# Kernel tuning notes

Hardware: AMD Instinct MI355X
Metric: run time of the kernel (lower is better)

## Reference

```python
import jax, jax.numpy as jnp
import numpy as np

V, L, H, D = 2048, 16, 8, 64   # vocab, max_chars, n_head, word_vec_d
B = 8192                        # number of words in batch (rows of char_code)
NW_TOTAL = 8192                 # len(word_code)
N_NAMES = 2048                  # total names (4 words each)
N_GROUPS = 8                    # groups of names (256 each)
PAD = 0
TEMP = D ** 0.5
LN_EPS = 1e-5


def make_pos():
    freq = D // 2
    inv = 1.0 / np.power(10000.0, np.arange(freq) / freq)
    ph = np.outer(np.arange(L), inv)
    return jnp.asarray(np.hstack([np.cos(ph), np.sin(ph)]).astype(np.float32))


def setup_inputs() -> dict:
    key = jax.random.key(0)
    ks = jax.random.split(key, 8)
    char_emb = jax.random.normal(ks[0], (V, D), jnp.float32) * 0.02
    char_emb = char_emb.at[PAD].set(0.0)  # padding_idx row
    Wc = jax.random.normal(ks[1], (D, 3 * H * D), jnp.float32) * 0.02
    bc = jnp.zeros((3 * H * D,), jnp.float32)
    Wp = jax.random.normal(ks[2], (D, 3 * H * D), jnp.float32) * 0.02
    bp = jnp.zeros((3 * H * D,), jnp.float32)
    gamma = jnp.ones((D,), jnp.float32)
    beta = jnp.zeros((D,), jnp.float32)
    W1 = jax.random.normal(ks[3], (H, 16), jnp.float32) * 0.1
    b1 = jnp.zeros((16,), jnp.float32)
    W2 = jax.random.normal(ks[4], (16, 8), jnp.float32) * 0.1
    b2 = jnp.zeros((8,), jnp.float32)
    char_code = jax.random.randint(ks[5], (B, L), 1, V)
    char_code = char_code.at[::4, -2:].set(PAD)  # some padded tails
    word_code = jax.random.randint(ks[6], (NW_TOTAL,), 0, B)
    n_words = np.full((N_NAMES,), NW_TOTAL // N_NAMES, dtype=np.int64)
    n_names = np.full((N_GROUPS,), N_NAMES // N_GROUPS, dtype=np.int64)
    return {"char_emb": char_emb, "Wc": Wc, "bc": bc, "Wp": Wp, "bp": bp,
            "gamma": gamma, "beta": beta, "W1": W1, "b1": b1, "W2": W2, "b2": b2,
            "char_code": char_code, "word_code": word_code,
            "n_words": n_words, "n_names": n_names}


def reference(char_emb, Wc, bc, Wp, bp, gamma, beta, W1, b1, W2, b2,
              char_code, word_code, n_words, n_names):
    pos = make_pos()
    # ComputeQKV: linear d -> 3*H*d, reshape [N,3,H,D]
    cqkv = (char_emb @ Wc + bc).reshape(V, 3, H, D)
    cq, ck, cv = cqkv[:, 0], cqkv[:, 1], cqkv[:, 2]        # [V,H,D]
    pqkv = (pos @ Wp + bp).reshape(L, 3, H, D)
    pq, pk, pv = pqkv[:, 0], pqkv[:, 1], pqkv[:, 2]        # [L,H,D]
    # precomputed score tables
    char_qk = jnp.einsum('xhd,yhd->hxy', cq, ck).at[:, :, PAD].set(-1e9)  # [H,V,V]
    pos_qk = jnp.einsum('xhd,yhd->hxy', pq, pk)                            # [H,L,L]
    # char_q@pos_k + (pos_q@char_k)^T summed over the first dim of char_pos_qk
    cp = jnp.einsum('vhd,lhd->hvl', cq, pk) + jnp.einsum('lhd,vhd->hvl', pq, ck)  # [H,V,L]
    code = char_code                                        # [B,L]
    # gather-assembled scores, no [H,B*L,V] intermediate
    sim = (char_qk[:, code[:, :, None], code[:, None, :]]   # [H,B,L,L]
           + cp[:, code]
           + pos_qk[:, None]) / TEMP
    attn = jax.nn.softmax(sim, axis=-1)                     # [H,B,L,L] (dropout=0)
    v = jnp.transpose(cv[code], (2, 0, 1, 3)) + pv.transpose(1, 0, 2)[:, None]  # [H,B,L,D]
    out = jnp.einsum('hbij,hbjd->bihd', attn, v)            # [B,L,H,D]
    mu = out.mean(-1, keepdims=True)
    var = out.var(-1, keepdims=True)
    out = (out - mu) / jnp.sqrt(var + LN_EPS) * gamma + beta  # LayerNorm(D)
    char_ft = jnp.transpose(out, (0, 2, 1, 3))              # [B,H,L,D]
    mask = (code != PAD)
    pooled = jnp.einsum('bl,bhld->bhd', mask.astype(out.dtype), char_ft) \
             / mask.sum(-1)[:, None, None]                  # masked mean over chars
    x = jnp.transpose(pooled, (0, 2, 1))                    # [B,D,H]
    x = jax.nn.relu(x @ W1 + b1) @ W2 + b2                  # MLP over head dim -> [B,D,8]
    word_ft = x.reshape(B, -1)[word_code]                   # [NW_TOTAL, D*8]
    nw = np.asarray(n_words)
    seg = jnp.asarray(np.repeat(np.arange(nw.size), nw))
    name_ft = jax.ops.segment_sum(word_ft, seg, num_segments=nw.size) \
              / jnp.asarray(nw, word_ft.dtype)[:, None]     # ragged mean -> [N_NAMES, D*8]
    splits = np.cumsum(np.asarray(n_names))[:-1]
    return tuple(jnp.split(name_ft, splits, axis=0))
```

## Files before the change

### kernel.cpp

```cpp
#include <hip/hip_runtime.h>
#include <hip/hip_bf16.h>
#include <math.h>

typedef __attribute__((ext_vector_type(8))) short bfrag;
typedef __attribute__((ext_vector_type(4))) float ffrag;
typedef __attribute__((ext_vector_type(4))) float f4v;

#define C3 1536
#define PS 24

__device__ __forceinline__ unsigned short f2bf(float f) {
    unsigned u = __float_as_uint(f);
    return (unsigned short)((u + 0x7FFFu + ((u >> 16) & 1u)) >> 16);
}
__device__ __forceinline__ float bf2f(unsigned short s) {
    return __uint_as_float(((unsigned)s) << 16);
}

__global__ __launch_bounds__(256) void precompute_kernel(
    const float* __restrict__ char_emb, const float* __restrict__ Wc, const float* __restrict__ bc,
    const float* __restrict__ Wp, const float* __restrict__ bp,
    unsigned short* __restrict__ cqkv, float* __restrict__ pqkv,
    unsigned short* __restrict__ pbf)
{
    const int b = blockIdx.x;
    const int t = threadIdx.x;
    if (b < 1536) {
        const int mt = b / 6;
        const int nt = b - mt * 6;
        const int m0 = mt * 8;
        const int c = nt * 256 + t;
        const float bias = bc[c];
        float acc[8];
        #pragma unroll
        for (int r = 0; r < 8; ++r) acc[r] = bias;
        #pragma unroll 16
        for (int dd = 0; dd < 64; ++dd) {
            const float wv = Wc[dd * C3 + c];
            #pragma unroll
            for (int r = 0; r < 8; ++r)
                acc[r] = fmaf(char_emb[(m0 + r) * 64 + dd], wv, acc[r]);
        }
        #pragma unroll
        for (int r = 0; r < 8; ++r)
            cqkv[(size_t)(m0 + r) * C3 + c] = f2bf(acc[r]);
    } else {
        const int l = b - 1536;
        __shared__ float spos[64];
        if (t < 64) {
            const int f = t & 31;
            const float inv = exp2f(-(float)f * 0.41524101186092034f);
            const float ph = (float)l * inv;
            spos[t] = (t < 32) ? cosf(ph) : sinf(ph);
        }
        __syncthreads();
        #pragma unroll
        for (int cc = 0; cc < 6; ++cc) {
            const int c = t + cc * 256;
            float acc = bp[c];
            #pragma unroll
            for (int dd = 0; dd < 64; ++dd)
                acc = fmaf(spos[dd], Wp[dd * C3 + c], acc);
            pqkv[l * C3 + c] = acc;
            if (c < 1024)
                pbf[(c >> 6) * 1024 + l * 64 + (c & 63)] = f2bf(acc);
        }
    }
}

__global__ __launch_bounds__(256) void vprime_kernel(
    const unsigned short* __restrict__ cqkv, const float* __restrict__ pqkv,
    unsigned short* __restrict__ vtab)
{
    const int c = blockIdx.x;
    const int t = threadIdx.x;
    const int hd8 = t & 63;
    const int l0 = t >> 6;
    const bfrag cv = *(const bfrag*)(cqkv + (size_t)c * C3 + 1024 + hd8 * 8);
    #pragma unroll
    for (int li = 0; li < 4; ++li) {
        const int l = l0 + li * 4;
        const f4v pa = *(const f4v*)(pqkv + l * C3 + 1024 + hd8 * 8);
        const f4v pb = *(const f4v*)(pqkv + l * C3 + 1024 + hd8 * 8 + 4);
        bfrag o;
        #pragma unroll
        for (int j = 0; j < 8; ++j)
            o[j] = (short)f2bf(bf2f((unsigned short)cv[j]) + ((j < 4) ? pa[j] : pb[j - 4]));
        *(bfrag*)(vtab + ((size_t)c * 16 + l) * 512 + hd8 * 8) = o;
    }
}

__global__ __launch_bounds__(256, 8) void attn_kernel(
    const unsigned short* __restrict__ cqkv, const unsigned short* __restrict__ pbf,
    const unsigned short* __restrict__ vtab, const int* __restrict__ char_code,
    const float* __restrict__ gamma, const float* __restrict__ beta,
    float* __restrict__ pooled)
{
    __shared__ __attribute__((aligned(16))) unsigned short sVt[4 * 1024];
    __shared__ __attribute__((aligned(16))) unsigned short sP[4 * 16 * PS];

    const int t = threadIdx.x;
    const int lane = t & 63;
    const int wid = t >> 6;
    const int gw = blockIdx.x * 4 + wid;
    const int w = gw >> 3;
    const int h = gw & 7;
    const int quad = lane >> 4;
    const int n = lane & 15;

    const int code = char_code[w * 16 + n];
    const bool kvalid = (code != 0);
    const unsigned long long msk = __ballot(kvalid);
    const int nv = __popcll(msk & 0xFFFFull);

    float gam[4], bet[4];
    #pragma unroll
    for (int dt = 0; dt < 4; ++dt) {
        gam[dt] = gamma[dt * 16 + n];
        bet[dt] = beta[dt * 16 + n];
    }

    unsigned short* vt = sVt + wid * 1024;
    #pragma unroll
    for (int cc = 0; cc < 2; ++cc) {
        const int d8 = quad + cc * 4;
        const bfrag vb = *(const bfrag*)(vtab + ((size_t)code * 16 + n) * 512 + h * 64 + d8 * 8);
        #pragma unroll
        for (int j = 0; j < 8; ++j) {
            const int d = d8 * 8 + j;
            const int e = ((d >> 4) * 2 + (n >> 3)) * 128
                        + ((d & 15) ^ ((n >> 3) << 2)) * 8 + (n & 7);
            vt[e] = (unsigned short)vb[j];
        }
    }

    ffrag accS = {0.f, 0.f, 0.f, 0.f};
    {
        const unsigned short* cbase = cqkv + (size_t)code * C3 + h * 64;
        const unsigned short* pq = pbf + h * 1024 + n * 64;
        const unsigned short* pk = pbf + (8 + h) * 1024 + n * 64;
        #pragma unroll
        for (int cc = 0; cc < 2; ++cc) {
            const int off = quad * 8 + cc * 32;
            const bfrag cqF = *(const bfrag*)(cbase + off);
            const bfrag ckF = *(const bfrag*)(cbase + 512 + off);
            const bfrag pqF = *(const bfrag*)(pq + off);
            const bfrag pkF = *(const bfrag*)(pk + off);
            accS = __builtin_amdgcn_mfma_f32_16x16x32_bf16(cqF, ckF, accS, 0, 0, 0);
            accS = __builtin_amdgcn_mfma_f32_16x16x32_bf16(cqF, pkF, accS, 0, 0, 0);
            accS = __builtin_amdgcn_mfma_f32_16x16x32_bf16(pqF, pkF, accS, 0, 0, 0);
            accS = __builtin_amdgcn_mfma_f32_16x16x32_bf16(ckF, pqF, accS, 0, 0, 0);
        }
    }

    float sv[4], mx[4], pr[4], sm[4];
    #pragma unroll
    for (int r = 0; r < 4; ++r) sv[r] = kvalid ? accS[r] * 0.125f : -1e30f;
    #pragma unroll
    for (int r = 0; r < 4; ++r) mx[r] = sv[r];
    #pragma unroll
    for (int xm = 1; xm <= 8; xm <<= 1) {
        #pragma unroll
        for (int r = 0; r < 4; ++r) mx[r] = fmaxf(mx[r], __shfl_xor(mx[r], xm));
    }
    #pragma unroll
    for (int r = 0; r < 4; ++r) { pr[r] = __expf(sv[r] - mx[r]); sm[r] = pr[r]; }
    #pragma unroll
    for (int xm = 1; xm <= 8; xm <<= 1) {
        #pragma unroll
        for (int r = 0; r < 4; ++r) sm[r] += __shfl_xor(sm[r], xm);
    }
    unsigned short* pt = sP + wid * 16 * PS;
    #pragma unroll
    for (int r = 0; r < 4; ++r)
        pt[(quad * 4 + r) * PS + n] = f2bf(pr[r] * __builtin_amdgcn_rcpf(sm[r]));

    bfrag ap;
    #pragma unroll
    for (int j = 0; j < 8; ++j) ap[j] = 0;
    if (quad < 2) ap = *(const bfrag*)(pt + n * PS + quad * 8);
    const int q2 = quad & 1;
    ffrag accO[4];
    #pragma unroll
    for (int dt = 0; dt < 4; ++dt) { ffrag z = {0.f,0.f,0.f,0.f}; accO[dt] = z; }
    #pragma unroll
    for (int dt = 0; dt < 4; ++dt) {
        const bfrag bv = *(const bfrag*)(vt + (dt * 2 + q2) * 128 + (n ^ (q2 << 2)) * 8);
        accO[dt] = __builtin_amdgcn_mfma_f32_16x16x32_bf16(ap, bv, accO[dt], 0, 0, 0);
    }

    float ps1[4], ps2[4];
    #pragma unroll
    for (int r = 0; r < 4; ++r) {
        ps1[r] = accO[0][r] + accO[1][r] + accO[2][r] + accO[3][r];
        ps2[r] = accO[0][r]*accO[0][r] + accO[1][r]*accO[1][r]
               + accO[2][r]*accO[2][r] + accO[3][r]*accO[3][r];
    }
    #pragma unroll
    for (int xm = 1; xm <= 8; xm <<= 1) {
        #pragma unroll
        for (int r = 0; r < 4; ++r) {
            ps1[r] += __shfl_xor(ps1[r], xm);
            ps2[r] += __shfl_xor(ps2[r], xm);
        }
    }
    float pool[4] = {0.f, 0.f, 0.f, 0.f};
    #pragma unroll
    for (int r = 0; r < 4; ++r) {
        const float mu   = ps1[r] * 0.015625f;
        const float var  = fmaxf(ps2[r] * 0.015625f - mu * mu, 0.f);
        const float rstd = rsqrtf(var + 1e-5f);
        const float iv = ((msk >> (quad * 4 + r)) & 1ull) ? 1.f : 0.f;
        #pragma unroll
        for (int dt = 0; dt < 4; ++dt)
            pool[dt] += iv * fmaf((accO[dt][r] - mu) * rstd, gam[dt], bet[dt]);
    }
    #pragma unroll
    for (int xm = 16; xm <= 32; xm <<= 1) {
        #pragma unroll
        for (int dt = 0; dt < 4; ++dt) pool[dt] += __shfl_xor(pool[dt], xm);
    }
    if (quad == 0) {
        const float invnv = 1.f / (float)nv;
        #pragma unroll
        for (int dt = 0; dt < 4; ++dt)
            pooled[(size_t)w * 512 + h * 64 + dt * 16 + n] = pool[dt] * invnv;
    }
}

__global__ __launch_bounds__(256) void scan_kernel(const int* __restrict__ n_words,
                                                   int* __restrict__ offsets)
{
    __shared__ int part[256];
    const int t = threadIdx.x;
    int loc[8];
    int s = 0;
    #pragma unroll
    for (int r = 0; r < 8; ++r) { loc[r] = s; s += n_words[t * 8 + r]; }
    part[t] = s;
    __syncthreads();
    for (int off = 1; off < 256; off <<= 1) {
        const int u = (t >= off) ? part[t - off] : 0;
        __syncthreads();
        part[t] += u;
        __syncthreads();
    }
    const int excl = (t == 0) ? 0 : part[t - 1];
    #pragma unroll
    for (int r = 0; r < 8; ++r) offsets[t * 8 + r] = excl + loc[r];
}

__global__ __launch_bounds__(128) void mlp_avg_kernel(
    const float* __restrict__ pooled, const int* __restrict__ word_code,
    const int* __restrict__ n_words, const int* __restrict__ offsets,
    const float* __restrict__ W1, const float* __restrict__ b1,
    const float* __restrict__ W2, const float* __restrict__ b2,
    float* __restrict__ out)
{
    __shared__ float sPool[512];
    __shared__ float sHid[64 * 17];
    __shared__ float sWb[280];
    const int nm = blockIdx.x;
    const int t = threadIdx.x;
    sWb[t] = W1[t];
    sWb[144 + t] = W2[t];
    if (t < 16) sWb[128 + t] = b1[t];
    if (t < 8)  sWb[272 + t] = b2[t];

    const int off = offsets[nm];
    const int cnt = n_words[nm];
    const int d = t & 63, o4 = (t >> 6) * 4;
    float xacc[4] = {0.f, 0.f, 0.f, 0.f};

    for (int r = 0; r < cnt; ++r) {
        const int wc = word_code[off + r];
        __syncthreads();
        *(f4v*)(sPool + t * 4) = *(const f4v*)(pooled + (size_t)wc * 512 + t * 4);
        __syncthreads();
        if (t < 64) {
            float pl[8];
            #pragma unroll
            for (int hh = 0; hh < 8; ++hh) pl[hh] = sPool[hh * 64 + t];
            #pragma unroll
            for (int c = 0; c < 16; ++c) {
                float hs = sWb[128 + c];
                #pragma unroll
                for (int hh = 0; hh < 8; ++hh) hs = fmaf(pl[hh], sWb[hh * 16 + c], hs);
                sHid[t * 17 + c] = fmaxf(hs, 0.f);
            }
        }
        __syncthreads();
        #pragma unroll
        for (int c = 0; c < 16; ++c) {
            const float hc = sHid[d * 17 + c];
            #pragma unroll
            for (int oo = 0; oo < 4; ++oo)
                xacc[oo] = fmaf(hc, sWb[144 + c * 8 + o4 + oo], xacc[oo]);
        }
    }
    const float inv = 1.f / (float)cnt;
    f4v res;
    #pragma unroll
    for (int oo = 0; oo < 4; ++oo) res[oo] = xacc[oo] * inv + sWb[272 + o4 + oo];
    *(f4v*)(out + (size_t)nm * 512 + d * 8 + o4) = res;
}

extern "C" void kernel_launch(void* const* d_in, const int* in_sizes, int n_in,
                              void* d_out, int out_size, void* d_ws, size_t ws_size,
                              hipStream_t stream) {
    (void)in_sizes; (void)n_in; (void)out_size; (void)ws_size;
    const float* char_emb = (const float*)d_in[0];
    const float* Wc    = (const float*)d_in[1];
    const float* bc    = (const float*)d_in[2];
    const float* Wp    = (const float*)d_in[3];
    const float* bp    = (const float*)d_in[4];
    const float* gamma = (const float*)d_in[5];
    const float* beta  = (const float*)d_in[6];
    const float* W1    = (const float*)d_in[7];
    const float* b1    = (const float*)d_in[8];
    const float* W2    = (const float*)d_in[9];
    const float* b2    = (const float*)d_in[10];
    const int* char_code = (const int*)d_in[11];
    const int* word_code = (const int*)d_in[12];
    const int* n_words   = (const int*)d_in[13];

    char* ws = (char*)d_ws;
    unsigned short* cqkv = (unsigned short*)ws;
    float* pqkv = (float*)(ws + 6291456);
    unsigned short* pbf  = (unsigned short*)(ws + 6389760);
    unsigned short* vtab = (unsigned short*)(ws + 6422528);
    float* pooled = (float*)(ws + 39976960);
    int* offsets  = (int*)(ws + 56754176);
    float* out = (float*)d_out;

    precompute_kernel<<<1552, 256, 0, stream>>>(char_emb, Wc, bc, Wp, bp, cqkv, pqkv, pbf);
    vprime_kernel<<<2048, 256, 0, stream>>>(cqkv, pqkv, vtab);
    attn_kernel<<<16384, 256, 0, stream>>>(cqkv, pbf, vtab, char_code, gamma, beta, pooled);
    scan_kernel<<<1, 256, 0, stream>>>(n_words, offsets);
    mlp_avg_kernel<<<2048, 128, 0, stream>>>(pooled, word_code, n_words, offsets,
                                             W1, b1, W2, b2, out);
}
```

Before: 210.0 us.

## Fold softmax scale into Q, drop max/normalise, DPP reductions, remove scan kernel

Result: faster. 204.5 us (-2.6%).

```diff
diff --git a/kernel.cpp b/kernel.cpp
--- a/kernel.cpp
+++ b/kernel.cpp
@@ -15,6 +15,19 @@
 }
 __device__ __forceinline__ float bf2f(unsigned short s) {
     return __uint_as_float(((unsigned)s) << 16);
+}
+
+__device__ __forceinline__ float row16_sum(float x) {
+    int v;
+    v = __builtin_amdgcn_update_dpp(0, __float_as_int(x), 0xB1, 0xF, 0xF, true);
+    x += __int_as_float(v);
+    v = __builtin_amdgcn_update_dpp(0, __float_as_int(x), 0x4E, 0xF, 0xF, true);
+    x += __int_as_float(v);
+    v = __builtin_amdgcn_update_dpp(0, __float_as_int(x), 0x124, 0xF, 0xF, true);
+    x += __int_as_float(v);
+    v = __builtin_amdgcn_update_dpp(0, __float_as_int(x), 0x128, 0xF, 0xF, true);
+    x += __int_as_float(v);
+    return x;
 }
 
 __global__ __launch_bounds__(256) void precompute_kernel(
@@ -30,6 +43,7 @@
         const int nt = b - mt * 6;
         const int m0 = mt * 8;
         const int c = nt * 256 + t;
+        const float qs = (c < 512) ? 0.125f : 1.f;
         const float bias = bc[c];
         float acc[8];
         #pragma unroll
@@ -43,7 +57,7 @@
         }
         #pragma unroll
         for (int r = 0; r < 8; ++r)
-            cqkv[(size_t)(m0 + r) * C3 + c] = f2bf(acc[r]);
+            cqkv[(size_t)(m0 + r) * C3 + c] = f2bf(acc[r] * qs);
     } else {
         const int l = b - 1536;
         __shared__ float spos[64];
@@ -62,8 +76,10 @@
             for (int dd = 0; dd < 64; ++dd)
                 acc = fmaf(spos[dd], Wp[dd * C3 + c], acc);
             pqkv[l * C3 + c] = acc;
-            if (c < 1024)
-                pbf[(c >> 6) * 1024 + l * 64 + (c & 63)] = f2bf(acc);
+            if (c < 1024) {
+                const float qs = (c < 512) ? 0.125f : 1.f;
+                pbf[(c >> 6) * 1024 + l * 64 + (c & 63)] = f2bf(acc * qs);
+            }
         }
     }
 }
@@ -153,27 +169,16 @@
         }
     }
 
-    float sv[4], mx[4], pr[4], sm[4];
-    #pragma unroll
-    for (int r = 0; r < 4; ++r) sv[r] = kvalid ? accS[r] * 0.125f : -1e30f;
-    #pragma unroll
-    for (int r = 0; r < 4; ++r) mx[r] = sv[r];
-    #pragma unroll
-    for (int xm = 1; xm <= 8; xm <<= 1) {
-        #pragma unroll
-        for (int r = 0; r < 4; ++r) mx[r] = fmaxf(mx[r], __shfl_xor(mx[r], xm));
-    }
-    #pragma unroll
-    for (int r = 0; r < 4; ++r) { pr[r] = __expf(sv[r] - mx[r]); sm[r] = pr[r]; }
-    #pragma unroll
-    for (int xm = 1; xm <= 8; xm <<= 1) {
-        #pragma unroll
-        for (int r = 0; r < 4; ++r) sm[r] += __shfl_xor(sm[r], xm);
+    float pr[4], sm[4];
+    #pragma unroll
+    for (int r = 0; r < 4; ++r) {
+        pr[r] = kvalid ? __expf(accS[r]) : 0.f;
+        sm[r] = row16_sum(pr[r]);
     }
     unsigned short* pt = sP + wid * 16 * PS;
     #pragma unroll
     for (int r = 0; r < 4; ++r)
-        pt[(quad * 4 + r) * PS + n] = f2bf(pr[r] * __builtin_amdgcn_rcpf(sm[r]));
+        pt[(quad * 4 + r) * PS + n] = f2bf(pr[r]);
 
     bfrag ap;
     #pragma unroll
@@ -195,21 +200,15 @@
         ps1[r] = accO[0][r] + accO[1][r] + accO[2][r] + accO[3][r];
         ps2[r] = accO[0][r]*accO[0][r] + accO[1][r]*accO[1][r]
                + accO[2][r]*accO[2][r] + accO[3][r]*accO[3][r];
-    }
-    #pragma unroll
-    for (int xm = 1; xm <= 8; xm <<= 1) {
-        #pragma unroll
-        for (int r = 0; r < 4; ++r) {
-            ps1[r] += __shfl_xor(ps1[r], xm);
-            ps2[r] += __shfl_xor(ps2[r], xm);
-        }
+        ps1[r] = row16_sum(ps1[r]);
+        ps2[r] = row16_sum(ps2[r]);
     }
     float pool[4] = {0.f, 0.f, 0.f, 0.f};
     #pragma unroll
     for (int r = 0; r < 4; ++r) {
         const float mu   = ps1[r] * 0.015625f;
         const float var  = fmaxf(ps2[r] * 0.015625f - mu * mu, 0.f);
-        const float rstd = rsqrtf(var + 1e-5f);
+        const float rstd = rsqrtf(var + sm[r] * sm[r] * 1e-5f);
         const float iv = ((msk >> (quad * 4 + r)) & 1ull) ? 1.f : 0.f;
         #pragma unroll
         for (int dt = 0; dt < 4; ++dt)
@@ -222,37 +221,16 @@
     }
     if (quad == 0) {
         const float invnv = 1.f / (float)nv;
-        #pragma unroll
-        for (int dt = 0; dt < 4; ++dt)
-            pooled[(size_t)w * 512 + h * 64 + dt * 16 + n] = pool[dt] * invnv;
-    }
-}
-
-__global__ __launch_bounds__(256) void scan_kernel(const int* __restrict__ n_words,
-                                                   int* __restrict__ offsets)
-{
-    __shared__ int part[256];
-    const int t = threadIdx.x;
-    int loc[8];
-    int s = 0;
-    #pragma unroll
-    for (int r = 0; r < 8; ++r) { loc[r] = s; s += n_words[t * 8 + r]; }
-    part[t] = s;
-    __syncthreads();
-    for (int off = 1; off < 256; off <<= 1) {
-        const int u = (t >= off) ? part[t - off] : 0;
-        __syncthreads();
-        part[t] += u;
-        __syncthreads();
-    }
-    const int excl = (t == 0) ? 0 : part[t - 1];
-    #pragma unroll
-    for (int r = 0; r < 8; ++r) offsets[t * 8 + r] = excl + loc[r];
+        f4v o;
+        #pragma unroll
+        for (int dt = 0; dt < 4; ++dt) o[dt] = pool[dt] * invnv;
+        *(f4v*)(pooled + (size_t)w * 512 + h * 64 + n * 4) = o;
+    }
 }
 
 __global__ __launch_bounds__(128) void mlp_avg_kernel(
     const float* __restrict__ pooled, const int* __restrict__ word_code,
-    const int* __restrict__ n_words, const int* __restrict__ offsets,
+    const int* __restrict__ n_words,
     const float* __restrict__ W1, const float* __restrict__ b1,
     const float* __restrict__ W2, const float* __restrict__ b2,
     float* __restrict__ out)
@@ -260,6 +238,7 @@
     __shared__ float sPool[512];
     __shared__ float sHid[64 * 17];
     __shared__ float sWb[280];
+    __shared__ int sred[128];
     const int nm = blockIdx.x;
     const int t = threadIdx.x;
     sWb[t] = W1[t];
@@ -267,9 +246,19 @@
     if (t < 16) sWb[128 + t] = b1[t];
     if (t < 8)  sWb[272 + t] = b2[t];
 
-    const int off = offsets[nm];
+    int part = 0;
+    for (int i = t; i < nm; i += 128) part += n_words[i];
+    sred[t] = part;
+    __syncthreads();
+    for (int s = 64; s > 0; s >>= 1) {
+        if (t < s) sred[t] += sred[t + s];
+        __syncthreads();
+    }
+    const int off = sred[0];
     const int cnt = n_words[nm];
+
     const int d = t & 63, o4 = (t >> 6) * 4;
+    const int dmap = (d & 15) * 4 + (d >> 4);
     float xacc[4] = {0.f, 0.f, 0.f, 0.f};
 
     for (int r = 0; r < cnt; ++r) {
@@ -280,7 +269,7 @@
         if (t < 64) {
             float pl[8];
             #pragma unroll
-            for (int hh = 0; hh < 8; ++hh) pl[hh] = sPool[hh * 64 + t];
+            for (int hh = 0; hh < 8; ++hh) pl[hh] = sPool[hh * 64 + dmap];
             #pragma unroll
             for (int c = 0; c < 16; ++c) {
                 float hs = sWb[128 + c];
@@ -330,13 +319,11 @@
     unsigned short* pbf  = (unsigned short*)(ws + 6389760);
     unsigned short* vtab = (unsigned short*)(ws + 6422528);
     float* pooled = (float*)(ws + 39976960);
-    int* offsets  = (int*)(ws + 56754176);
     float* out = (float*)d_out;
 
     precompute_kernel<<<1552, 256, 0, stream>>>(char_emb, Wc, bc, Wp, bp, cqkv, pqkv, pbf);
     vprime_kernel<<<2048, 256, 0, stream>>>(cqkv, pqkv, vtab);
     attn_kernel<<<16384, 256, 0, stream>>>(cqkv, pbf, vtab, char_code, gamma, beta, pooled);
-    scan_kernel<<<1, 256, 0, stream>>>(n_words, offsets);
-    mlp_avg_kernel<<<2048, 128, 0, stream>>>(pooled, word_code, n_words, offsets,
+    mlp_avg_kernel<<<2048, 128, 0, stream>>>(pooled, word_code, n_words,
                                              W1, b1, W2, b2, out);
 }
```
